# Performance work log

Hardware: AMD Instinct MI355X
Metric: run time of the kernel (lower is better)

Reference implementation:

```python
import jax, jax.numpy as jnp
import numpy as np
import math

HIDDEN = 1024
N_HEADS = 16
HEAD_DIM = HIDDEN // N_HEADS

def _safe(x, clamp_val):
    x = jnp.nan_to_num(x, nan=0.0, posinf=0.0, neginf=0.0)
    return jnp.clip(x, -clamp_val, clamp_val)

def _stable_linear(x, W, b):
    # StableLinear: clamp(50) -> linear -> clamp(50)
    x = _safe(x, 50.0)
    out = x @ W.T + b
    return _safe(out, 50.0)

def setup_inputs() -> dict:
    key = jax.random.key(0)
    ks = jax.random.split(key, 12)
    bsz, q_len, kv_len = 4, 1024, 2048
    q = jax.random.normal(ks[0], (bsz, q_len, HIDDEN), dtype=jnp.float32)
    kv = jax.random.normal(ks[1], (bsz, kv_len, HIDDEN), dtype=jnp.float32)
    key_padding_mask = jax.random.bernoulli(ks[2], 0.1, (bsz, kv_len))
    bound = 1.0 / math.sqrt(HIDDEN)
    def mk_w(k):
        return jax.random.uniform(k, (HIDDEN, HIDDEN), jnp.float32, -bound, bound)
    def mk_b(k):
        return jax.random.uniform(k, (HIDDEN,), jnp.float32, -bound, bound)
    return {
        'q': q, 'kv': kv, 'key_padding_mask': key_padding_mask,
        'Wq': mk_w(ks[3]), 'bq': mk_b(ks[4]),
        'Wk': mk_w(ks[5]), 'bk': mk_b(ks[6]),
        'Wv': mk_w(ks[7]), 'bv': mk_b(ks[8]),
        'Wo': mk_w(ks[9]), 'bo': mk_b(ks[10]),
    }

def reference(q, kv, key_padding_mask, Wq, bq, Wk, bk, Wv, bv, Wo, bo):
    bsz, q_len, _ = q.shape
    kv_len = kv.shape[1]
    # outer _safe(50) then StableLinear's own _safe(50) (idempotent)
    qh = _stable_linear(_safe(q, 50.0), Wq, bq)
    kh = _stable_linear(_safe(kv, 50.0), Wk, bk)
    vh = _stable_linear(_safe(kv, 50.0), Wv, bv)
    # [b, h, s, d]
    qh = qh.reshape(bsz, q_len, N_HEADS, HEAD_DIM).transpose(0, 2, 1, 3)
    kh = kh.reshape(bsz, kv_len, N_HEADS, HEAD_DIM).transpose(0, 2, 1, 3)
    vh = vh.reshape(bsz, kv_len, N_HEADS, HEAD_DIM).transpose(0, 2, 1, 3)
    scores = jnp.einsum('bhqd,bhkd->bhqk', qh.astype(jnp.float32), kh.astype(jnp.float32))
    scores = scores / math.sqrt(HEAD_DIM)
    scores = jnp.clip(scores, -80.0, 80.0)
    scores = jnp.where(key_padding_mask[:, None, None, :], -10000.0, scores)
    attn = jax.nn.softmax(scores, axis=-1)  # dropout is identity in eval mode
    out = jnp.einsum('bhqk,bhkd->bhqd', attn, vh.astype(jnp.float32))
    out = out.transpose(0, 2, 1, 3).reshape(bsz, q_len, HIDDEN)
    out = _stable_linear(_safe(out, 50.0), Wo, bo)
    return _safe(out, 50.0)
```

## Files before the change

kernel.cpp:

```cpp
#include <hip/hip_runtime.h>
#include <hip/hip_bf16.h>
#include <stdint.h>
#include <math.h>

#define HIDDEN 1024
#define NHEADS 16
#define HDIM   64
#define BSZ    4
#define QLEN   1024
#define KVLEN  2048

typedef __bf16 bf16_t;
typedef __bf16 bf16x8 __attribute__((ext_vector_type(8)));
typedef __bf16 bf16x4 __attribute__((ext_vector_type(4)));
typedef float  f32x4  __attribute__((ext_vector_type(4)));

#define C_SCALE 0.18033688f
#define C_FMADD (-43.2808512f)

#define GLOAD16(g, l) \
    __builtin_amdgcn_global_load_lds((const __attribute__((address_space(1))) void*)(g), \
                                     (__attribute__((address_space(3))) void*)(l), 16, 0, 0)

__device__ __forceinline__ float clamp50(float v) {
    return fminf(fmaxf(v, -50.f), 50.f);
}

#define NW4  ((HIDDEN * HIDDEN) / 4)
#define NWCVT (4 * NW4 / 256)

__global__ void cvt_w_mask_kernel(const float* __restrict__ W0, const float* __restrict__ W1,
                                  const float* __restrict__ W2, const float* __restrict__ W3,
                                  bf16_t* __restrict__ w_bf,
                                  const void* __restrict__ msk, float* __restrict__ maskadd) {
    if (blockIdx.x >= NWCVT) {
        __shared__ int s_float, s_multi;
        const int t = threadIdx.x;
        if (t == 0) { s_float = 0; s_multi = 0; }
        __syncthreads();
        const uint32_t* w = (const uint32_t*)msk;
        int cf = 0, cm = 0;
        for (int i = t; i < 2048; i += 256) {
            uint32_t v = w[i];
            if (v == 0x3F800000u) cf++;
            else if (v & 0xFFFFFF00u) cm++;
        }
        if (cf) atomicAdd(&s_float, cf);
        if (cm) atomicAdd(&s_multi, cm);
        __syncthreads();
        const int mode = (s_float > 0) ? 2 : ((s_multi > 0) ? 0 : 1);
        const int base = (blockIdx.x - NWCVT) * 2048;
        for (int i = base + t; i < base + 2048; i += 256) {
            bool m;
            if (mode == 2)      m = ((const float*)msk)[i] != 0.0f;
            else if (mode == 1) m = ((const int*)msk)[i] != 0;
            else                m = ((const unsigned char*)msk)[i] != 0;
            maskadd[i] = m ? (-100000.0f + C_FMADD) : C_FMADD;
        }
        return;
    }
    const int i = blockIdx.x * blockDim.x + threadIdx.x;
    const int ws = i >> 18, off = i & (NW4 - 1);
    const float* W = (ws == 0) ? W0 : (ws == 1) ? W1 : (ws == 2) ? W2 : W3;
    const float4 v = ((const float4*)W)[off];
    bf16x4 o;
    o[0] = (bf16_t)clamp50(v.x); o[1] = (bf16_t)clamp50(v.y);
    o[2] = (bf16_t)clamp50(v.z); o[3] = (bf16_t)clamp50(v.w);
    ((bf16x4*)w_bf)[(size_t)ws * NW4 + off] = o;
}

__device__ __forceinline__ void proj_core(const char* __restrict__ Ab,
                                          const char* __restrict__ Bb,
                                          char* Ls, f32x4 (&acc)[4][2],
                                          int wave, int lane, int wm, int wn)
{
    constexpr int BUF = 256 * 128;
    const int srcsw = ((lane & 7) ^ (lane >> 3)) << 4;
    const int rowl = lane >> 3;
    const int ql = lane & 15;

    float4 a0[2], a1[2];
#pragma unroll
    for (int i = 0; i < 2; ++i) {
        const int row = i * 64 + wave * 8 + rowl;
        const float4* p = (const float4*)(Ab + (size_t)row * (HIDDEN * 4) + (srcsw << 1));
        a0[i] = p[0]; a1[i] = p[1];
    }
#pragma unroll
    for (int i = 0; i < 2; ++i) {
        const int row = i * 64 + wave * 8 + rowl;
        GLOAD16(Bb + (size_t)row * (HIDDEN * 2) + srcsw,
                Ls + 16384 + i * 8192 + wave * 1024);
    }
#pragma unroll
    for (int i = 0; i < 2; ++i) {
        bf16x8 o;
        o[0] = (bf16_t)clamp50(a0[i].x); o[1] = (bf16_t)clamp50(a0[i].y);
        o[2] = (bf16_t)clamp50(a0[i].z); o[3] = (bf16_t)clamp50(a0[i].w);
        o[4] = (bf16_t)clamp50(a1[i].x); o[5] = (bf16_t)clamp50(a1[i].y);
        o[6] = (bf16_t)clamp50(a1[i].z); o[7] = (bf16_t)clamp50(a1[i].w);
        *(bf16x8*)(Ls + i * 8192 + wave * 1024 + lane * 16) = o;
    }
    __syncthreads();

    for (int kt = 0; kt < HIDDEN / 64; ++kt) {
        const int cur = kt & 1;
        if (kt < HIDDEN / 64 - 1) {
#pragma unroll
            for (int i = 0; i < 2; ++i) {
                const int row = i * 64 + wave * 8 + rowl;
                const float4* p = (const float4*)(Ab + (size_t)row * (HIDDEN * 4)
                                                  + (kt + 1) * 256 + (srcsw << 1));
                a0[i] = p[0]; a1[i] = p[1];
            }
#pragma unroll
            for (int i = 0; i < 2; ++i) {
                const int row = i * 64 + wave * 8 + rowl;
                GLOAD16(Bb + (size_t)row * (HIDDEN * 2) + (kt + 1) * 128 + srcsw,
                        Ls + (cur ^ 1) * BUF + 16384 + i * 8192 + wave * 1024);
            }
        }
        const char* Abase = Ls + cur * BUF;
        const char* Bbase = Abase + 16384;
#pragma unroll
        for (int kc = 0; kc < 2; ++kc) {
            const int kbyte = kc * 64 + ((lane >> 4) << 4);
            bf16x8 af[4], bfr[2];
#pragma unroll
            for (int f2 = 0; f2 < 4; ++f2) {
                const int arow = wm * 64 + f2 * 16 + ql;
                af[f2] = *(const bf16x8*)(Abase + arow * 128 + (kbyte ^ ((arow & 7) << 4)));
            }
#pragma unroll
            for (int f2 = 0; f2 < 2; ++f2) {
                const int brow = wn * 32 + f2 * 16 + ql;
                bfr[f2] = *(const bf16x8*)(Bbase + brow * 128 + (kbyte ^ ((brow & 7) << 4)));
            }
#pragma unroll
            for (int mf = 0; mf < 4; ++mf)
#pragma unroll
                for (int nf = 0; nf < 2; ++nf)
                    acc[mf][nf] = __builtin_amdgcn_mfma_f32_16x16x32_bf16(af[mf], bfr[nf], acc[mf][nf], 0, 0, 0);
        }
        if (kt < HIDDEN / 64 - 1) {
#pragma unroll
            for (int i = 0; i < 2; ++i) {
                bf16x8 o;
                o[0] = (bf16_t)clamp50(a0[i].x); o[1] = (bf16_t)clamp50(a0[i].y);
                o[2] = (bf16_t)clamp50(a0[i].z); o[3] = (bf16_t)clamp50(a0[i].w);
                o[4] = (bf16_t)clamp50(a1[i].x); o[5] = (bf16_t)clamp50(a1[i].y);
                o[6] = (bf16_t)clamp50(a1[i].z); o[7] = (bf16_t)clamp50(a1[i].w);
                *(bf16x8*)(Ls + (cur ^ 1) * BUF + i * 8192 + wave * 1024 + lane * 16) = o;
            }
        }
        __syncthreads();
    }
}

template <int NF>
__device__ __forceinline__ void epi_head(f32x4 (&acc)[4][NF], const float* bias,
                                         bf16_t* out, int m0, int n0, int slog,
                                         int wm, int wn, int lane)
{
#pragma unroll
    for (int mf = 0; mf < 4; ++mf) {
#pragma unroll
        for (int nf = 0; nf < NF; ++nf) {
            const int gn = n0 + wn * (NF * 16) + nf * 16 + (lane & 15);
            const float bv = bias[gn];
#pragma unroll
            for (int r = 0; r < 4; ++r) {
                const int gm = m0 + wm * 64 + mf * 16 + ((lane >> 4) << 2) + r;
                const float v = clamp50(acc[mf][nf][r] + bv);
                const int b = gm >> slog;
                const int s = gm & ((1 << slog) - 1);
                const int h = gn >> 6, d = gn & 63;
                out[((((size_t)(b * NHEADS + h)) << slog) + s) * HDIM + d] = (bf16_t)v;
            }
        }
    }
}

__global__ __launch_bounds__(512)
void gemm_proj_all(const float* __restrict__ qf32, const float* __restrict__ kvf32,
                   const bf16_t* __restrict__ w_bf,
                   const float* __restrict__ bq, const float* __restrict__ bk,
                   const float* __restrict__ bv,
                   bf16_t* __restrict__ qh, bf16_t* __restrict__ kh,
                   bf16_t* __restrict__ vt)
{
    __shared__ __align__(16) bf16_t Smem[2 * 256 * 64];

    const int bid = blockIdx.x;
    const int lid = (bid & 7) * 160 + (bid >> 3);

    int seg, j;
    if (lid < 256)      { seg = 0; j = lid; }
    else if (lid < 768) { seg = 1; j = lid - 256; }
    else                { seg = 2; j = lid - 768; }
    const int m0 = (j >> 3) * 128;
    const int n0 = (j & 7) * 128;
    const float*  A    = (seg == 0) ? qf32 : kvf32;
    const bf16_t* B    = w_bf + (size_t)seg * (HIDDEN * HIDDEN);
    const float*  bias = (seg == 0) ? bq : (seg == 1) ? bk : bv;

    const int t = threadIdx.x;
    const int wave = t >> 6, lane = t & 63;
    const int wm = wave >> 2, wn = wave & 3;

    f32x4 acc[4][2] = {};
    proj_core((const char*)A + (size_t)m0 * (HIDDEN * 4),
              (const char*)B + (size_t)n0 * (HIDDEN * 2),
              (char*)Smem, acc, wave, lane, wm, wn);

    if (seg == 0) {
        epi_head<2>(acc, bias, qh, m0, n0, 10, wm, wn, lane);
        return;
    }
    if (seg == 1) {
        epi_head<2>(acc, bias, kh, m0, n0, 11, wm, wn, lane);
        return;
    }

    bf16_t* Cls = Smem;
    const int dl = t >> 2;
    const int sh = (t & 3) << 4;
    const int gn = n0 + dl;
    const int h = gn >> 6, d = gn & 63;
    const int bb = m0 >> 11;
    bf16_t* dst = vt + ((size_t)((bb * NHEADS + h) * HDIM + d)) * KVLEN
                + (m0 & (KVLEN - 1)) + sh;
    __syncthreads();
#pragma unroll
    for (int ph = 0; ph < 2; ++ph) {
        if (wm == ph) {
#pragma unroll
            for (int mf = 0; mf < 4; ++mf) {
#pragma unroll
                for (int nf = 0; nf < 2; ++nf) {
                    const int dcol = wn * 32 + nf * 16 + (lane & 15);
                    const float bv2 = bias[n0 + dcol];
#pragma unroll
                    for (int r = 0; r < 4; ++r) {
                        const int srow = mf * 16 + ((lane >> 4) << 2) + r;
                        Cls[srow * 130 + dcol] = (bf16_t)clamp50(acc[mf][nf][r] + bv2);
                    }
                }
            }
        }
        __syncthreads();
#pragma unroll
        for (int j0 = 0; j0 < 16; j0 += 8) {
            bf16x8 v;
#pragma unroll
            for (int jj = 0; jj < 8; ++jj) v[jj] = Cls[(sh + j0 + jj) * 130 + dl];
            *(bf16x8*)(dst + ph * 64 + j0) = v;
        }
        __syncthreads();
    }
}

template <int NT>
__device__ __forceinline__ void stage_tile8(const char* __restrict__ Ab,
                                            const char* __restrict__ Bb,
                                            char* base, int kt, int wave, int rowl, int srcsw)
{
#pragma unroll
    for (int i = 0; i < 2; ++i) {
        const int row = i * 64 + wave * 8 + rowl;
        GLOAD16(Ab + (size_t)row * (HIDDEN * 2) + kt * 128 + srcsw,
                base + i * 8192 + wave * 1024);
    }
#pragma unroll
    for (int i = 0; i < NT / 64; ++i) {
        const int row = i * 64 + wave * 8 + rowl;
        GLOAD16(Bb + (size_t)row * (HIDDEN * 2) + kt * 128 + srcsw,
                base + 16384 + i * 8192 + wave * 1024);
    }
}

template <int NT>
__device__ __forceinline__ void gemm_core_db8(const char* __restrict__ Ab,
                                              const char* __restrict__ Bb,
                                              char* Ls,
                                              f32x4 (&acc)[4][NT / 64],
                                              int wave, int lane, int wm, int wn)
{
    constexpr int NFB = NT / 64;
    constexpr int BUF = (128 + NT) * 128;
    const int srcsw = ((lane & 7) ^ (lane >> 3)) << 4;
    const int rowl = lane >> 3;
    const int ql = lane & 15;

    stage_tile8<NT>(Ab, Bb, Ls, 0, wave, rowl, srcsw);
    __syncthreads();

    for (int kt = 0; kt < HIDDEN / 64; ++kt) {
        const int cur = kt & 1;
        if (kt < HIDDEN / 64 - 1)
            stage_tile8<NT>(Ab, Bb, Ls + (cur ^ 1) * BUF, kt + 1, wave, rowl, srcsw);
        const char* Abase = Ls + cur * BUF;
        const char* Bbase = Abase + 16384;
#pragma unroll
        for (int kc = 0; kc < 2; ++kc) {
            const int kbyte = kc * 64 + ((lane >> 4) << 4);
            bf16x8 af[4], bfr[NFB];
#pragma unroll
            for (int f2 = 0; f2 < 4; ++f2) {
                const int arow = wm * 64 + f2 * 16 + ql;
                af[f2] = *(const bf16x8*)(Abase + arow * 128 + (kbyte ^ ((arow & 7) << 4)));
            }
#pragma unroll
            for (int f2 = 0; f2 < NFB; ++f2) {
                const int brow = wn * (NT / 4) + f2 * 16 + ql;
                bfr[f2] = *(const bf16x8*)(Bbase + brow * 128 + (kbyte ^ ((brow & 7) << 4)));
            }
#pragma unroll
            for (int mf = 0; mf < 4; ++mf)
#pragma unroll
                for (int nf = 0; nf < NFB; ++nf)
                    acc[mf][nf] = __builtin_amdgcn_mfma_f32_16x16x32_bf16(af[mf], bfr[nf], acc[mf][nf], 0, 0, 0);
        }
        __syncthreads();
    }
}

__global__ __launch_bounds__(512)
void gemm_out_kernel(const bf16_t* __restrict__ A, const bf16_t* __restrict__ B,
                     const float* __restrict__ bias, float* __restrict__ out)
{
    constexpr int NT = 64;
    __shared__ __align__(16) bf16_t Smem[2 * (128 + NT) * 64];

    const int bid = blockIdx.x;
    const int lid = (bid & 7) * 64 + (bid >> 3);
    const int m0 = (lid >> 4) * 128;
    const int n0 = (lid & 15) * NT;
    const int t = threadIdx.x;
    const int wave = t >> 6, lane = t & 63;
    const int wm = wave >> 2, wn = wave & 3;

    f32x4 acc[4][1] = {};
    gemm_core_db8<NT>((const char*)A + (size_t)m0 * (HIDDEN * 2),
                      (const char*)B + (size_t)n0 * (HIDDEN * 2),
                      (char*)Smem, acc, wave, lane, wm, wn);

#pragma unroll
    for (int mf = 0; mf < 4; ++mf) {
        const int gn = n0 + wn * 16 + (lane & 15);
        const float bv = bias[gn];
#pragma unroll
        for (int r = 0; r < 4; ++r) {
            const int gm = m0 + wm * 64 + mf * 16 + ((lane >> 4) << 2) + r;
            out[(size_t)gm * HIDDEN + gn] = clamp50(acc[mf][0][r] + bv);
        }
    }
}

__global__ __launch_bounds__(512)
void attn_fwd_kernel(const bf16_t* __restrict__ Qh, const bf16_t* __restrict__ Kh,
                     const bf16_t* __restrict__ Vt, const float* __restrict__ maskadd,
                     bf16_t* __restrict__ aout)
{
    __shared__ __align__(16) bf16_t Kls[2][64 * 64];
    __shared__ __align__(16) bf16_t Vls[2][64 * 64];
    __shared__ __align__(16) float Cbuf[4][32 * 64];
    __shared__ float Lbuf[4][2][16];

    const int f = blockIdx.x;
    const int o = (f & 7) * 64 + (f >> 3);
    const int qt = o & 7;
    const int bh = o >> 3;
    const int b = bh >> 4, h = bh & 15;
    const int t = threadIdx.x, wave = t >> 6, lane = t & 63;
    const int wq = wave & 3;
    const int wg = wave >> 2;
    const int g = lane >> 4, ql = lane & 15;

    const int qbase = qt * 128 + wq * 32;
    bf16x8 qf[2][2];
#pragma unroll
    for (int qq = 0; qq < 2; ++qq) {
        const bf16_t* qp = Qh + ((size_t)bh * QLEN + qbase + qq * 16 + ql) * HDIM + (g << 3);
        qf[qq][0] = *(const bf16x8*)qp;
        qf[qq][1] = *(const bf16x8*)(qp + 32);
    }

    f32x4 oacc[2][4] = {};
    float lsum[2] = {0.f, 0.f};

    const int srcsw = ((lane & 7) ^ (lane >> 3)) << 4;
    const int R = wave * 8 + (lane >> 3);
    const int kap = 32 * (R >> 5) + 8 * ((R >> 2) & 3) + 4 * ((R >> 4) & 1) + (R & 3);

    const char* Kb = (const char*)(Kh + (size_t)bh * KVLEN * HDIM);
    const char* Vb = (const char*)(Vt + (size_t)bh * HDIM * KVLEN);
    const float* mrow = maskadd + b * KVLEN + wg * 32 + g * 8;
    const int kb0 = g << 4;
    const int vcol = wg * 64 + kb0;

    GLOAD16(Kb + (size_t)kap * 128 + srcsw, (char*)&Kls[0][0] + wave * 1024);
    GLOAD16(Vb + (size_t)R * (KVLEN * 2) + srcsw, (char*)&Vls[0][0] + wave * 1024);
    f32x4 madd_c[2], madd_n[2];
    madd_c[0] = *(const f32x4*)(mrow);
    madd_c[1] = *(const f32x4*)(mrow + 4);
    __syncthreads();

    for (int kt = 0; kt < KVLEN / 64; ++kt) {
        const int cur = kt & 1;
        if (kt < KVLEN / 64 - 1) {
            const size_t ko = (size_t)(kt + 1) * 8192;
            GLOAD16(Kb + ko + (size_t)kap * 128 + srcsw,
                    (char*)&Kls[cur ^ 1][0] + wave * 1024);
            GLOAD16(Vb + (size_t)R * (KVLEN * 2) + (size_t)(kt + 1) * 128 + srcsw,
                    (char*)&Vls[cur ^ 1][0] + wave * 1024);
            madd_n[0] = *(const f32x4*)(mrow + (kt + 1) * 64);
            madd_n[1] = *(const f32x4*)(mrow + (kt + 1) * 64 + 4);
        }
        const char* Kc = (const char*)&Kls[cur][0];
        const char* Vc = (const char*)&Vls[cur][0];

        f32x4 sacc[2][2] = {};
        __builtin_amdgcn_s_setprio(1);
#pragma unroll
        for (int kb = 0; kb < 2; ++kb) {
            const int key = wg * 32 + kb * 16 + ql;
            const int rowoff = key * 128;
            const int sw = (key & 7) << 4;
            const bf16x8 kf0 = *(const bf16x8*)(Kc + rowoff + ((kb0)      ^ sw));
            const bf16x8 kf1 = *(const bf16x8*)(Kc + rowoff + ((kb0 + 64) ^ sw));
#pragma unroll
            for (int qq = 0; qq < 2; ++qq) {
                sacc[qq][kb] = __builtin_amdgcn_mfma_f32_16x16x32_bf16(kf0, qf[qq][0], sacc[qq][kb], 0, 0, 0);
                sacc[qq][kb] = __builtin_amdgcn_mfma_f32_16x16x32_bf16(kf1, qf[qq][1], sacc[qq][kb], 0, 0, 0);
            }
        }
        __builtin_amdgcn_s_setprio(0);

        bf16x8 pa[2];
#pragma unroll
        for (int qq = 0; qq < 2; ++qq) {
            float pv[2][4];
            float ls = 0.f;
#pragma unroll
            for (int kb = 0; kb < 2; ++kb) {
#pragma unroll
                for (int r = 0; r < 4; ++r) {
                    pv[kb][r] = __builtin_amdgcn_exp2f(
                        __builtin_fmaf(sacc[qq][kb][r], C_SCALE, madd_c[kb][r]));
                    ls += pv[kb][r];
                }
            }
            lsum[qq] += ls;
#pragma unroll
            for (int r = 0; r < 4; ++r) {
                pa[qq][r]     = (bf16_t)pv[0][r];
                pa[qq][4 + r] = (bf16_t)pv[1][r];
            }
        }

        __builtin_amdgcn_s_setprio(1);
#pragma unroll
        for (int db = 0; db < 4; ++db) {
            const int vrow = db * 16 + ql;
            const int vsw = (vrow & 7) << 4;
            const bf16x8 vf = *(const bf16x8*)(Vc + vrow * 128 + (vcol ^ vsw));
#pragma unroll
            for (int qq = 0; qq < 2; ++qq)
                oacc[qq][db] = __builtin_amdgcn_mfma_f32_16x16x32_bf16(pa[qq], vf, oacc[qq][db], 0, 0, 0);
        }
        __builtin_amdgcn_s_setprio(0);

        __syncthreads();
#pragma unroll
        for (int kb = 0; kb < 2; ++kb) madd_c[kb] = madd_n[kb];
    }

#pragma unroll
    for (int qq = 0; qq < 2; ++qq) {
        float l = lsum[qq];
        l += __shfl_xor(l, 16);
        l += __shfl_xor(l, 32);
        lsum[qq] = l;
    }
    const int rbase = g << 2;
    if (wg == 1) {
#pragma unroll
        for (int qq = 0; qq < 2; ++qq) {
#pragma unroll
            for (int db = 0; db < 4; ++db)
#pragma unroll
                for (int r = 0; r < 4; ++r)
                    Cbuf[wq][(qq * 16 + rbase + r) * 64 + db * 16 + ql] = oacc[qq][db][r];
            if (lane < 16) Lbuf[wq][qq][lane] = lsum[qq];
        }
    }
    __syncthreads();
    if (wg == 0) {
#pragma unroll
        for (int qq = 0; qq < 2; ++qq) {
            const float Lq = lsum[qq] + Lbuf[wq][qq][ql];
#pragma unroll
            for (int r = 0; r < 4; ++r) {
                const float Lr = __shfl(Lq, rbase + r);
                const float inv = 1.0f / Lr;
                const int qrow = qbase + qq * 16 + rbase + r;
                bf16_t* orow = aout + ((size_t)(b * QLEN + qrow)) * HIDDEN + h * HDIM;
#pragma unroll
                for (int db = 0; db < 4; ++db) {
                    const float add = Cbuf[wq][(qq * 16 + rbase + r) * 64 + db * 16 + ql];
                    orow[db * 16 + ql] = (bf16_t)((oacc[qq][db][r] + add) * inv);
                }
            }
        }
    }
}

extern "C" void kernel_launch(void* const* d_in, const int* in_sizes, int n_in,
                              void* d_out, int out_size, void* d_ws, size_t ws_size,
                              hipStream_t stream) {
    (void)in_sizes; (void)n_in; (void)out_size; (void)ws_size;
    const float* q   = (const float*)d_in[0];
    const float* kv  = (const float*)d_in[1];
    const void*  msk = d_in[2];
    const float* Wq  = (const float*)d_in[3];
    const float* bq  = (const float*)d_in[4];
    const float* Wk  = (const float*)d_in[5];
    const float* bk  = (const float*)d_in[6];
    const float* Wv  = (const float*)d_in[7];
    const float* bv  = (const float*)d_in[8];
    const float* Wo  = (const float*)d_in[9];
    const float* bo  = (const float*)d_in[10];

    char* ws = (char*)d_ws;
    const size_t MB = 1024 * 1024;
    float*  maskadd = (float*)ws;
    bf16_t* w_bf  = (bf16_t*)(ws + 32 * 1024);
    bf16_t* aout  = (bf16_t*)(ws + 32 * 1024 + 8  * MB);
    bf16_t* qh    = (bf16_t*)(ws + 32 * 1024 + 32 * MB);
    bf16_t* kh    = (bf16_t*)(ws + 32 * 1024 + 40 * MB);
    bf16_t* vt    = (bf16_t*)(ws + 32 * 1024 + 56 * MB);

    bf16_t* wo_bf = w_bf + (size_t)3 * HIDDEN * HIDDEN;

    cvt_w_mask_kernel<<<dim3(NWCVT + 4), 256, 0, stream>>>(
        Wq, Wk, Wv, Wo, w_bf, msk, maskadd);

    gemm_proj_all<<<dim3(1280), 512, 0, stream>>>(
        q, kv, w_bf, bq, bk, bv, qh, kh, vt);

    attn_fwd_kernel<<<dim3(512), 512, 0, stream>>>(qh, kh, vt, maskadd, aout);

    gemm_out_kernel<<<dim3(512), 512, 0, stream>>>(aout, wo_bf, bo, (float*)d_out);
}
```

Baseline: 140.0 us.

## Deepen projection GEMM A-operand prefetch to two tiles ahead with register ping-pong

Restructures the projection GEMM main loop so the fp32 A tile is loaded from global memory two k-steps ahead into alternating register sets. The loop is unrolled by two so the register sets swap roles. The convert-and-write of the next tile to LDS, and the B global-to-LDS load, are issued before the MFMA compute instead of after it. This hides more global load latency behind compute, at the cost of extra VGPRs for the second fp32 staging set, which could lower occupancy.

```diff
diff --git a/kernel.cpp b/kernel.cpp
--- a/kernel.cpp
+++ b/kernel.cpp
@@ -69,6 +69,55 @@
     ((bf16x4*)w_bf)[(size_t)ws * NW4 + off] = o;
 }
 
+#define PROJ_CVT_WRITE(dstbuf, wr0, wr1) \
+    _Pragma("unroll") for (int i_ = 0; i_ < 2; ++i_) { \
+        bf16x8 o_; \
+        o_[0] = (bf16_t)clamp50(wr0[i_].x); o_[1] = (bf16_t)clamp50(wr0[i_].y); \
+        o_[2] = (bf16_t)clamp50(wr0[i_].z); o_[3] = (bf16_t)clamp50(wr0[i_].w); \
+        o_[4] = (bf16_t)clamp50(wr1[i_].x); o_[5] = (bf16_t)clamp50(wr1[i_].y); \
+        o_[6] = (bf16_t)clamp50(wr1[i_].z); o_[7] = (bf16_t)clamp50(wr1[i_].w); \
+        *(bf16x8*)((dstbuf) + i_ * 8192 + wave * 1024 + lane * 16) = o_; \
+    }
+
+#define PROJ_BODY(kt, wr0, wr1, ld0, ld1) do { \
+    const int cur_ = (kt) & 1; \
+    char* nbuf_ = Ls + (cur_ ^ 1) * BUF; \
+    if ((kt) < 15) { \
+        PROJ_CVT_WRITE(nbuf_, wr0, wr1) \
+        _Pragma("unroll") for (int i_ = 0; i_ < 2; ++i_) { \
+            const int row_ = i_ * 64 + wave * 8 + rowl; \
+            GLOAD16(Bb + (size_t)row_ * (HIDDEN * 2) + ((kt) + 1) * 128 + srcsw, \
+                    nbuf_ + 16384 + i_ * 8192 + wave * 1024); \
+        } \
+    } \
+    if ((kt) < 14) { \
+        _Pragma("unroll") for (int i_ = 0; i_ < 2; ++i_) { \
+            const int row_ = i_ * 64 + wave * 8 + rowl; \
+            const float4* p_ = (const float4*)(Ab + (size_t)row_ * (HIDDEN * 4) \
+                                               + ((kt) + 2) * 256 + (srcsw << 1)); \
+            ld0[i_] = p_[0]; ld1[i_] = p_[1]; \
+        } \
+    } \
+    const char* Abase_ = Ls + cur_ * BUF; \
+    const char* Bbase_ = Abase_ + 16384; \
+    _Pragma("unroll") for (int kc_ = 0; kc_ < 2; ++kc_) { \
+        const int kbyte_ = kc_ * 64 + ((lane >> 4) << 4); \
+        bf16x8 af_[4], bfr_[2]; \
+        _Pragma("unroll") for (int f_ = 0; f_ < 4; ++f_) { \
+            const int arow_ = wm * 64 + f_ * 16 + ql; \
+            af_[f_] = *(const bf16x8*)(Abase_ + arow_ * 128 + (kbyte_ ^ ((arow_ & 7) << 4))); \
+        } \
+        _Pragma("unroll") for (int f_ = 0; f_ < 2; ++f_) { \
+            const int brow_ = wn * 32 + f_ * 16 + ql; \
+            bfr_[f_] = *(const bf16x8*)(Bbase_ + brow_ * 128 + (kbyte_ ^ ((brow_ & 7) << 4))); \
+        } \
+        _Pragma("unroll") for (int mf_ = 0; mf_ < 4; ++mf_) \
+            _Pragma("unroll") for (int nf_ = 0; nf_ < 2; ++nf_) \
+                acc[mf_][nf_] = __builtin_amdgcn_mfma_f32_16x16x32_bf16(af_[mf_], bfr_[nf_], acc[mf_][nf_], 0, 0, 0); \
+    } \
+    __syncthreads(); \
+} while (0)
+
 __device__ __forceinline__ void proj_core(const char* __restrict__ Ab,
                                           const char* __restrict__ Bb,
                                           char* Ls, f32x4 (&acc)[4][2],
@@ -79,81 +128,28 @@
     const int rowl = lane >> 3;
     const int ql = lane & 15;
 
-    float4 a0[2], a1[2];
+    float4 e0[2], e1[2], f0[2], f1[2];
+
 #pragma unroll
     for (int i = 0; i < 2; ++i) {
         const int row = i * 64 + wave * 8 + rowl;
         const float4* p = (const float4*)(Ab + (size_t)row * (HIDDEN * 4) + (srcsw << 1));
-        a0[i] = p[0]; a1[i] = p[1];
-    }
+        e0[i] = p[0]; e1[i] = p[1];
+        GLOAD16(Bb + (size_t)row * (HIDDEN * 2) + srcsw,
+                Ls + 16384 + i * 8192 + wave * 1024);
+    }
+    PROJ_CVT_WRITE(Ls, e0, e1)
 #pragma unroll
     for (int i = 0; i < 2; ++i) {
         const int row = i * 64 + wave * 8 + rowl;
-        GLOAD16(Bb + (size_t)row * (HIDDEN * 2) + srcsw,
-                Ls + 16384 + i * 8192 + wave * 1024);
-    }
-#pragma unroll
-    for (int i = 0; i < 2; ++i) {
-        bf16x8 o;
-        o[0] = (bf16_t)clamp50(a0[i].x); o[1] = (bf16_t)clamp50(a0[i].y);
-        o[2] = (bf16_t)clamp50(a0[i].z); o[3] = (bf16_t)clamp50(a0[i].w);
-        o[4] = (bf16_t)clamp50(a1[i].x); o[5] = (bf16_t)clamp50(a1[i].y);
-        o[6] = (bf16_t)clamp50(a1[i].z); o[7] = (bf16_t)clamp50(a1[i].w);
-        *(bf16x8*)(Ls + i * 8192 + wave * 1024 + lane * 16) = o;
+        const float4* p = (const float4*)(Ab + (size_t)row * (HIDDEN * 4) + 256 + (srcsw << 1));
+        e0[i] = p[0]; e1[i] = p[1];
     }
     __syncthreads();
 
-    for (int kt = 0; kt < HIDDEN / 64; ++kt) {
-        const int cur = kt & 1;
-        if (kt < HIDDEN / 64 - 1) {
-#pragma unroll
-            for (int i = 0; i < 2; ++i) {
-                const int row = i * 64 + wave * 8 + rowl;
-                const float4* p = (const float4*)(Ab + (size_t)row * (HIDDEN * 4)
-                                                  + (kt + 1) * 256 + (srcsw << 1));
-                a0[i] = p[0]; a1[i] = p[1];
-            }
-#pragma unroll
-            for (int i = 0; i < 2; ++i) {
-                const int row = i * 64 + wave * 8 + rowl;
-                GLOAD16(Bb + (size_t)row * (HIDDEN * 2) + (kt + 1) * 128 + srcsw,
-                        Ls + (cur ^ 1) * BUF + 16384 + i * 8192 + wave * 1024);
-            }
-        }
-        const char* Abase = Ls + cur * BUF;
-        const char* Bbase = Abase + 16384;
-#pragma unroll
-        for (int kc = 0; kc < 2; ++kc) {
-            const int kbyte = kc * 64 + ((lane >> 4) << 4);
-            bf16x8 af[4], bfr[2];
-#pragma unroll
-            for (int f2 = 0; f2 < 4; ++f2) {
-                const int arow = wm * 64 + f2 * 16 + ql;
-                af[f2] = *(const bf16x8*)(Abase + arow * 128 + (kbyte ^ ((arow & 7) << 4)));
-            }
-#pragma unroll
-            for (int f2 = 0; f2 < 2; ++f2) {
-                const int brow = wn * 32 + f2 * 16 + ql;
-                bfr[f2] = *(const bf16x8*)(Bbase + brow * 128 + (kbyte ^ ((brow & 7) << 4)));
-            }
-#pragma unroll
-            for (int mf = 0; mf < 4; ++mf)
-#pragma unroll
-                for (int nf = 0; nf < 2; ++nf)
-                    acc[mf][nf] = __builtin_amdgcn_mfma_f32_16x16x32_bf16(af[mf], bfr[nf], acc[mf][nf], 0, 0, 0);
-        }
-        if (kt < HIDDEN / 64 - 1) {
-#pragma unroll
-            for (int i = 0; i < 2; ++i) {
-                bf16x8 o;
-                o[0] = (bf16_t)clamp50(a0[i].x); o[1] = (bf16_t)clamp50(a0[i].y);
-                o[2] = (bf16_t)clamp50(a0[i].z); o[3] = (bf16_t)clamp50(a0[i].w);
-                o[4] = (bf16_t)clamp50(a1[i].x); o[5] = (bf16_t)clamp50(a1[i].y);
-                o[6] = (bf16_t)clamp50(a1[i].z); o[7] = (bf16_t)clamp50(a1[i].w);
-                *(bf16x8*)(Ls + (cur ^ 1) * BUF + i * 8192 + wave * 1024 + lane * 16) = o;
-            }
-        }
-        __syncthreads();
+    for (int kt2 = 0; kt2 < 8; ++kt2) {
+        PROJ_BODY(2 * kt2,     e0, e1, f0, f1);
+        PROJ_BODY(2 * kt2 + 1, f0, f1, e0, e1);
     }
 }
 
```

Result: faster. 136.9 us (-2.2%).

## Widen projection GEMM tile to 128x256 with single-buffered A staging

Applied to the files above, without the earlier changes.

The fused Q/K/V projection GEMM now uses 128x256 output tiles instead of 128x128, halving the grid to 640 blocks and doubling MFMA work per wave (4x4 fragments). Each fp32 activation tile is converted once per block, so redundant A loads and conversions across N tiles drop by half. To fit LDS, A is now single-buffered while B stays double-buffered, which adds an extra barrier per k-step. The V-transpose epilogue is adapted to the wider tile. Fewer blocks and higher register pressure may lower occupancy and CU load balance.

```diff
diff --git a/kernel.cpp b/kernel.cpp
--- a/kernel.cpp
+++ b/kernel.cpp
@@ -69,38 +69,44 @@
     ((bf16x4*)w_bf)[(size_t)ws * NW4 + off] = o;
 }
 
-__device__ __forceinline__ void proj_core(const char* __restrict__ Ab,
-                                          const char* __restrict__ Bb,
-                                          char* Ls, f32x4 (&acc)[4][2],
-                                          int wave, int lane, int wm, int wn)
-{
-    constexpr int BUF = 256 * 128;
+#define AOFF  0
+#define BOFF  16384
+#define BBUF  32768
+
+#define PROJ_CVT_WRITE_A(wr0, wr1) \
+    _Pragma("unroll") for (int i_ = 0; i_ < 2; ++i_) { \
+        bf16x8 o_; \
+        o_[0] = (bf16_t)clamp50(wr0[i_].x); o_[1] = (bf16_t)clamp50(wr0[i_].y); \
+        o_[2] = (bf16_t)clamp50(wr0[i_].z); o_[3] = (bf16_t)clamp50(wr0[i_].w); \
+        o_[4] = (bf16_t)clamp50(wr1[i_].x); o_[5] = (bf16_t)clamp50(wr1[i_].y); \
+        o_[6] = (bf16_t)clamp50(wr1[i_].z); o_[7] = (bf16_t)clamp50(wr1[i_].w); \
+        *(bf16x8*)(Ls + AOFF + i_ * 8192 + wave * 1024 + lane * 16) = o_; \
+    }
+
+__device__ __forceinline__ void proj_core3(const char* __restrict__ Ab,
+                                           const char* __restrict__ Bb,
+                                           char* Ls, f32x4 (&acc)[4][4],
+                                           int wave, int lane, int wm, int wn)
+{
     const int srcsw = ((lane & 7) ^ (lane >> 3)) << 4;
     const int rowl = lane >> 3;
     const int ql = lane & 15;
 
-    float4 a0[2], a1[2];
+    float4 e0[2], e1[2];
+
 #pragma unroll
     for (int i = 0; i < 2; ++i) {
         const int row = i * 64 + wave * 8 + rowl;
         const float4* p = (const float4*)(Ab + (size_t)row * (HIDDEN * 4) + (srcsw << 1));
-        a0[i] = p[0]; a1[i] = p[1];
-    }
-#pragma unroll
-    for (int i = 0; i < 2; ++i) {
+        e0[i] = p[0]; e1[i] = p[1];
+    }
+#pragma unroll
+    for (int i = 0; i < 4; ++i) {
         const int row = i * 64 + wave * 8 + rowl;
         GLOAD16(Bb + (size_t)row * (HIDDEN * 2) + srcsw,
-                Ls + 16384 + i * 8192 + wave * 1024);
-    }
-#pragma unroll
-    for (int i = 0; i < 2; ++i) {
-        bf16x8 o;
-        o[0] = (bf16_t)clamp50(a0[i].x); o[1] = (bf16_t)clamp50(a0[i].y);
-        o[2] = (bf16_t)clamp50(a0[i].z); o[3] = (bf16_t)clamp50(a0[i].w);
-        o[4] = (bf16_t)clamp50(a1[i].x); o[5] = (bf16_t)clamp50(a1[i].y);
-        o[6] = (bf16_t)clamp50(a1[i].z); o[7] = (bf16_t)clamp50(a1[i].w);
-        *(bf16x8*)(Ls + i * 8192 + wave * 1024 + lane * 16) = o;
-    }
+                Ls + BOFF + i * 8192 + wave * 1024);
+    }
+    PROJ_CVT_WRITE_A(e0, e1)
     __syncthreads();
 
     for (int kt = 0; kt < HIDDEN / 64; ++kt) {
@@ -111,47 +117,40 @@
                 const int row = i * 64 + wave * 8 + rowl;
                 const float4* p = (const float4*)(Ab + (size_t)row * (HIDDEN * 4)
                                                   + (kt + 1) * 256 + (srcsw << 1));
-                a0[i] = p[0]; a1[i] = p[1];
-            }
-#pragma unroll
-            for (int i = 0; i < 2; ++i) {
+                e0[i] = p[0]; e1[i] = p[1];
+            }
+#pragma unroll
+            for (int i = 0; i < 4; ++i) {
                 const int row = i * 64 + wave * 8 + rowl;
                 GLOAD16(Bb + (size_t)row * (HIDDEN * 2) + (kt + 1) * 128 + srcsw,
-                        Ls + (cur ^ 1) * BUF + 16384 + i * 8192 + wave * 1024);
-            }
-        }
-        const char* Abase = Ls + cur * BUF;
-        const char* Bbase = Abase + 16384;
+                        Ls + BOFF + (cur ^ 1) * BBUF + i * 8192 + wave * 1024);
+            }
+        }
+        const char* Abase = Ls + AOFF;
+        const char* Bbase = Ls + BOFF + cur * BBUF;
 #pragma unroll
         for (int kc = 0; kc < 2; ++kc) {
             const int kbyte = kc * 64 + ((lane >> 4) << 4);
-            bf16x8 af[4], bfr[2];
+            bf16x8 af[4], bfr[4];
 #pragma unroll
             for (int f2 = 0; f2 < 4; ++f2) {
                 const int arow = wm * 64 + f2 * 16 + ql;
                 af[f2] = *(const bf16x8*)(Abase + arow * 128 + (kbyte ^ ((arow & 7) << 4)));
             }
 #pragma unroll
-            for (int f2 = 0; f2 < 2; ++f2) {
-                const int brow = wn * 32 + f2 * 16 + ql;
+            for (int f2 = 0; f2 < 4; ++f2) {
+                const int brow = wn * 64 + f2 * 16 + ql;
                 bfr[f2] = *(const bf16x8*)(Bbase + brow * 128 + (kbyte ^ ((brow & 7) << 4)));
             }
 #pragma unroll
             for (int mf = 0; mf < 4; ++mf)
 #pragma unroll
-                for (int nf = 0; nf < 2; ++nf)
+                for (int nf = 0; nf < 4; ++nf)
                     acc[mf][nf] = __builtin_amdgcn_mfma_f32_16x16x32_bf16(af[mf], bfr[nf], acc[mf][nf], 0, 0, 0);
         }
+        __syncthreads();
         if (kt < HIDDEN / 64 - 1) {
-#pragma unroll
-            for (int i = 0; i < 2; ++i) {
-                bf16x8 o;
-                o[0] = (bf16_t)clamp50(a0[i].x); o[1] = (bf16_t)clamp50(a0[i].y);
-                o[2] = (bf16_t)clamp50(a0[i].z); o[3] = (bf16_t)clamp50(a0[i].w);
-                o[4] = (bf16_t)clamp50(a1[i].x); o[5] = (bf16_t)clamp50(a1[i].y);
-                o[6] = (bf16_t)clamp50(a1[i].z); o[7] = (bf16_t)clamp50(a1[i].w);
-                *(bf16x8*)(Ls + (cur ^ 1) * BUF + i * 8192 + wave * 1024 + lane * 16) = o;
-            }
+            PROJ_CVT_WRITE_A(e0, e1)
         }
         __syncthreads();
     }
@@ -181,7 +180,7 @@
     }
 }
 
-__global__ __launch_bounds__(512)
+__global__ __launch_bounds__(512, 4)
 void gemm_proj_all(const float* __restrict__ qf32, const float* __restrict__ kvf32,
                    const bf16_t* __restrict__ w_bf,
                    const float* __restrict__ bq, const float* __restrict__ bk,
@@ -189,17 +188,17 @@
                    bf16_t* __restrict__ qh, bf16_t* __restrict__ kh,
                    bf16_t* __restrict__ vt)
 {
-    __shared__ __align__(16) bf16_t Smem[2 * 256 * 64];
+    __shared__ __align__(16) char Smem[81920];
 
     const int bid = blockIdx.x;
-    const int lid = (bid & 7) * 160 + (bid >> 3);
+    const int lid = (bid & 7) * 80 + (bid >> 3);
 
     int seg, j;
-    if (lid < 256)      { seg = 0; j = lid; }
-    else if (lid < 768) { seg = 1; j = lid - 256; }
-    else                { seg = 2; j = lid - 768; }
-    const int m0 = (j >> 3) * 128;
-    const int n0 = (j & 7) * 128;
+    if (lid < 128)      { seg = 0; j = lid; }
+    else if (lid < 384) { seg = 1; j = lid - 128; }
+    else                { seg = 2; j = lid - 384; }
+    const int m0 = (j >> 2) * 128;
+    const int n0 = (j & 3) * 256;
     const float*  A    = (seg == 0) ? qf32 : kvf32;
     const bf16_t* B    = w_bf + (size_t)seg * (HIDDEN * HIDDEN);
     const float*  bias = (seg == 0) ? bq : (seg == 1) ? bk : bv;
@@ -208,28 +207,29 @@
     const int wave = t >> 6, lane = t & 63;
     const int wm = wave >> 2, wn = wave & 3;
 
-    f32x4 acc[4][2] = {};
-    proj_core((const char*)A + (size_t)m0 * (HIDDEN * 4),
-              (const char*)B + (size_t)n0 * (HIDDEN * 2),
-              (char*)Smem, acc, wave, lane, wm, wn);
+    f32x4 acc[4][4] = {};
+    proj_core3((const char*)A + (size_t)m0 * (HIDDEN * 4),
+               (const char*)B + (size_t)n0 * (HIDDEN * 2),
+               (char*)Smem, acc, wave, lane, wm, wn);
 
     if (seg == 0) {
-        epi_head<2>(acc, bias, qh, m0, n0, 10, wm, wn, lane);
+        epi_head<4>(acc, bias, qh, m0, n0, 10, wm, wn, lane);
         return;
     }
     if (seg == 1) {
-        epi_head<2>(acc, bias, kh, m0, n0, 11, wm, wn, lane);
+        epi_head<4>(acc, bias, kh, m0, n0, 11, wm, wn, lane);
         return;
     }
 
-    bf16_t* Cls = Smem;
-    const int dl = t >> 2;
-    const int sh = (t & 3) << 4;
+    bf16_t* Cls = (bf16_t*)Smem;
+    const int dl = t >> 1;
+    const int sh = (t & 1) << 5;
     const int gn = n0 + dl;
     const int h = gn >> 6, d = gn & 63;
     const int bb = m0 >> 11;
     bf16_t* dst = vt + ((size_t)((bb * NHEADS + h) * HDIM + d)) * KVLEN
                 + (m0 & (KVLEN - 1)) + sh;
+    const int rbase = (lane >> 4) << 2;
     __syncthreads();
 #pragma unroll
     for (int ph = 0; ph < 2; ++ph) {
@@ -237,23 +237,23 @@
 #pragma unroll
             for (int mf = 0; mf < 4; ++mf) {
 #pragma unroll
-                for (int nf = 0; nf < 2; ++nf) {
-                    const int dcol = wn * 32 + nf * 16 + (lane & 15);
+                for (int nf = 0; nf < 4; ++nf) {
+                    const int dcol = wn * 64 + nf * 16 + (lane & 15);
                     const float bv2 = bias[n0 + dcol];
 #pragma unroll
                     for (int r = 0; r < 4; ++r) {
-                        const int srow = mf * 16 + ((lane >> 4) << 2) + r;
-                        Cls[srow * 130 + dcol] = (bf16_t)clamp50(acc[mf][nf][r] + bv2);
+                        const int srow = mf * 16 + rbase + r;
+                        Cls[srow * 258 + dcol] = (bf16_t)clamp50(acc[mf][nf][r] + bv2);
                     }
                 }
             }
         }
         __syncthreads();
 #pragma unroll
-        for (int j0 = 0; j0 < 16; j0 += 8) {
+        for (int j0 = 0; j0 < 32; j0 += 8) {
             bf16x8 v;
 #pragma unroll
-            for (int jj = 0; jj < 8; ++jj) v[jj] = Cls[(sh + j0 + jj) * 130 + dl];
+            for (int jj = 0; jj < 8; ++jj) v[jj] = Cls[(sh + j0 + jj) * 258 + dl];
             *(bf16x8*)(dst + ph * 64 + j0) = v;
         }
         __syncthreads();
@@ -546,7 +546,7 @@
     cvt_w_mask_kernel<<<dim3(NWCVT + 4), 256, 0, stream>>>(
         Wq, Wk, Wv, Wo, w_bf, msk, maskadd);
 
-    gemm_proj_all<<<dim3(1280), 512, 0, stream>>>(
+    gemm_proj_all<<<dim3(640), 512, 0, stream>>>(
         q, kv, w_bf, bq, bk, bv, qh, kh, vt);
 
     attn_fwd_kernel<<<dim3(512), 512, 0, stream>>>(qh, kh, vt, maskadd, aout);
```

New measurement: 140.0 us. No clear change (-0.0%).
